# Kernel tuning notes

Measured on AMD Instinct MI355X. Metric: run time of the kernel, lower is better.

Reference implementation:

```python
import jax, jax.numpy as jnp
import numpy as np

B, T, S = 4, 128, 8192
HID, NH, NKV, HD = 2560, 8, 4, 256
INTER = 10240
WINDOW = 1024
SOFTCAP = 50.0
SCALING = 256 ** -0.5  # query_pre_attn_scalar ** -0.5
EPS = 1e-6
NEG = -2.3819763e38  # large negative for masking (matches Gemma mask value)
ROPE_THETA = 10000.0


def _rmsnorm(x, w):
    xf = x.astype(jnp.float32)
    o = xf * jax.lax.rsqrt(jnp.mean(xf * xf, axis=-1, keepdims=True) + EPS)
    return (o * (1.0 + w.astype(jnp.float32))).astype(x.dtype)


def _rope(x, cos, sin):
    # split-half rotation, matching torch apply_rotary_emb (chunk->complex->mul)
    d2 = x.shape[-1] // 2
    x1, x2 = x[..., :d2], x[..., d2:]
    c = cos[None, :, None, :]  # [1,T,1,D/2]
    s = sin[None, :, None, :]
    return jnp.concatenate([x1 * c - x2 * s, x1 * s + x2 * c], axis=-1)


def setup_inputs() -> dict:
    key = jax.random.key(0)
    ks = jax.random.split(key, 14)
    hidden_states = jax.random.normal(ks[0], (B, T, HID), jnp.float32)
    kv_write_indices = jnp.arange(T, dtype=jnp.int32)
    k_cache = jnp.zeros((B, S, NKV, HD), jnp.float32)
    v_cache = jnp.zeros((B, S, NKV, HD), jnp.float32)
    # rotary tables for positions 0..T-1
    inv = 1.0 / (ROPE_THETA ** (np.arange(0, HD, 2)[: HD // 2].astype(np.float32) / HD))
    fr = np.outer(np.arange(T, dtype=np.float32), inv).astype(np.float32)
    freqs_cos = jnp.asarray(np.cos(fr))
    freqs_sin = jnp.asarray(np.sin(fr))
    # masks: query i sits at absolute position i; cache slots >= T are unwritten
    qpos = jnp.arange(T)[:, None]
    kpos = jnp.arange(S)[None, :]
    causal = kpos <= qpos
    local = causal & ((qpos - kpos) < WINDOW)
    mask = jnp.broadcast_to(jnp.where(causal, 0.0, NEG)[None, None], (B, 1, T, S)).astype(jnp.float32)
    local_mask = jnp.broadcast_to(jnp.where(local, 0.0, NEG)[None, None], (B, 1, T, S)).astype(jnp.float32)
    sc = 0.02
    w_qkv = sc * jax.random.normal(ks[1], ((NH + 2 * NKV) * HD, HID), jnp.float32)
    w_o = sc * jax.random.normal(ks[2], (HID, NH * HD), jnp.float32)
    q_norm_w = 0.1 * jax.random.normal(ks[3], (HD,), jnp.float32)
    k_norm_w = 0.1 * jax.random.normal(ks[4], (HD,), jnp.float32)
    in_ln_w = 0.1 * jax.random.normal(ks[5], (HID,), jnp.float32)
    post_attn_ln_w = 0.1 * jax.random.normal(ks[6], (HID,), jnp.float32)
    pre_ffw_ln_w = 0.1 * jax.random.normal(ks[7], (HID,), jnp.float32)
    post_ffw_ln_w = 0.1 * jax.random.normal(ks[8], (HID,), jnp.float32)
    w_gate = sc * jax.random.normal(ks[9], (INTER, HID), jnp.float32)
    w_up = sc * jax.random.normal(ks[10], (INTER, HID), jnp.float32)
    w_down = sc * jax.random.normal(ks[11], (HID, INTER), jnp.float32)
    return {
        "hidden_states": hidden_states, "freqs_cos": freqs_cos, "freqs_sin": freqs_sin,
        "kv_write_indices": kv_write_indices, "k_cache": k_cache, "v_cache": v_cache,
        "mask": mask, "local_mask": local_mask,
        "w_qkv": w_qkv, "w_o": w_o, "q_norm_w": q_norm_w, "k_norm_w": k_norm_w,
        "in_ln_w": in_ln_w, "post_attn_ln_w": post_attn_ln_w,
        "pre_ffw_ln_w": pre_ffw_ln_w, "post_ffw_ln_w": post_ffw_ln_w,
        "w_gate": w_gate, "w_up": w_up, "w_down": w_down,
    }


def reference(hidden_states, freqs_cos, freqs_sin, kv_write_indices, k_cache, v_cache,
              mask, local_mask, w_qkv, w_o, q_norm_w, k_norm_w, in_ln_w,
              post_attn_ln_w, pre_ffw_ln_w, post_ffw_ln_w, w_gate, w_up, w_down):
    b, t, _ = hidden_states.shape
    residual = hidden_states
    h = _rmsnorm(hidden_states, in_ln_w)
    qkv = h @ w_qkv.T
    q_sz, kv_sz = NH * HD, NKV * HD
    xq = qkv[..., :q_sz].reshape(b, t, NH, HD)
    xk = qkv[..., q_sz:q_sz + kv_sz].reshape(b, t, NKV, HD)
    xv = qkv[..., q_sz + kv_sz:].reshape(b, t, NKV, HD)
    xq = _rmsnorm(xq, q_norm_w)  # QK-norm
    xk = _rmsnorm(xk, k_norm_w)
    xq = _rope(xq, freqs_cos, freqs_sin)
    xk = _rope(xk, freqs_cos, freqs_sin)
    kc = k_cache.at[:, kv_write_indices].set(xk)  # index_copy_ on dim 1
    vc = v_cache.at[:, kv_write_indices].set(xv)
    g = NH // NKV
    q = (xq * SCALING).reshape(b, t, NKV, g, HD)
    # GQA without repeat_interleave: group dim g shares each kv head
    scores = jnp.einsum('btkgd,bskd->bkgts', q, kc)
    scores = SOFTCAP * jnp.tanh(scores / SOFTCAP)  # logit softcapping
    scores = scores + local_mask[:, :, None]  # LOCAL_SLIDING -> use local mask
    probs = jax.nn.softmax(scores.astype(jnp.float32), axis=-1).astype(q.dtype)
    attn = jnp.einsum('bkgts,bskd->btkgd', probs, vc).reshape(b, t, NH * HD)
    attn = attn @ w_o.T
    h = residual + _rmsnorm(attn, post_attn_ln_w)
    residual = h
    x = _rmsnorm(h, pre_ffw_ln_w)
    gate = jax.nn.gelu(x @ w_gate.T, approximate=True)
    mlp = (gate * (x @ w_up.T)) @ w_down.T
    return residual + _rmsnorm(mlp, post_ffw_ln_w)
```

## Files before the change

kernel.cpp:

```cpp
#include <hip/hip_runtime.h>
#include <hip/hip_bf16.h>

#define B_ 4
#define T_ 128
#define HID 2560
#define NH 8
#define NKV 4
#define HD 256
#define INTER 10240
#define MROWS 512
#define EPS 1e-6f

typedef float f32x4 __attribute__((ext_vector_type(4)));
typedef __bf16 bf16x8 __attribute__((ext_vector_type(8)));

__device__ __forceinline__ unsigned short f2bf(float f){
  unsigned int u = __builtin_bit_cast(unsigned int, f);
  u += 0x7fffu + ((u >> 16) & 1u);
  return (unsigned short)(u >> 16);
}
__device__ __forceinline__ float bf2f(unsigned short u){
  unsigned int x = ((unsigned int)u) << 16;
  return __builtin_bit_cast(float, x);
}
__device__ __forceinline__ unsigned int cvtpk(float lo, float hi){
  unsigned int r;
  asm("v_cvt_pk_bf16_f32 %0, %1, %2" : "=v"(r) : "v"(lo), "v"(hi));
  return r;
}

__device__ __forceinline__ float bsum256(float v, float* buf){
  #pragma unroll
  for (int o = 32; o; o >>= 1) v += __shfl_xor(v, o);
  __syncthreads();
  if ((threadIdx.x & 63) == 0) buf[threadIdx.x >> 6] = v;
  __syncthreads();
  return buf[0] + buf[1] + buf[2] + buf[3];
}

__global__ __launch_bounds__(256) void rms_in(
    const float* __restrict__ x, const float* __restrict__ w,
    unsigned short* __restrict__ out)
{
  __shared__ float buf[4];
  const int r = blockIdx.x, tid = threadIdx.x;
  const float* xp = x + (size_t)r * HID;
  float v[10]; float ss = 0.f;
  #pragma unroll
  for (int j = 0; j < 10; j++){ v[j] = xp[tid + j*256]; ss += v[j]*v[j]; }
  ss = bsum256(ss, buf);
  float s = rsqrtf(ss * (1.f/HID) + EPS);
  #pragma unroll
  for (int j = 0; j < 10; j++){
    int i = tid + j*256;
    out[(size_t)r*HID + i] = f2bf(v[j] * s * (1.f + w[i]));
  }
}

template<bool BF16OUT>
__global__ __launch_bounds__(256, 2) void gemm_big(
    const unsigned short* __restrict__ A,
    const float* __restrict__ B0,
    const float* __restrict__ B1,
    int n_hi,
    void* __restrict__ Cv,
    int N, int K, int klen)
{
  __shared__ unsigned short As[2][256][40];
  __shared__ unsigned short Bs[2][128][40];
  const int tid = threadIdx.x;
  const int bid = (blockIdx.x & 7) * ((int)gridDim.x >> 3) + (blockIdx.x >> 3);
  const int bm = (bid & 1) << 8;
  const int bn = (bid >> 1) << 7;
  const int k0 = blockIdx.y * klen;
  const int nt = klen >> 5;

  const int srow = tid >> 1, shalf = tid & 1;
  const size_t A128 = (size_t)128 * K;
  const unsigned short* ApG = A + (size_t)(bm + srow) * K + k0 + (shalf << 4);
  const float* Bb = (bn < n_hi) ? B0 : B1;
  const int bnr = (bn < n_hi) ? bn : (bn - n_hi);
  const float* BpG = Bb + (size_t)(bnr + srow) * K + k0 + (shalf << 4);

  const int wave = tid >> 6, lane = tid & 63;
  const int wm = (wave & 1) << 7;
  const int wn = (wave >> 1) << 6;
  const int fr = lane & 15, kq = lane >> 4;

  f32x4 acc[8][4];
  #pragma unroll
  for (int i = 0; i < 8; i++)
    #pragma unroll
    for (int j = 0; j < 4; j++)
      #pragma unroll
      for (int e = 0; e < 4; e++) acc[i][j][e] = 0.f;

  uint4  ra0 = *(const uint4*)(ApG);
  uint4  ra1 = *(const uint4*)(ApG + 8);
  uint4  ra2 = *(const uint4*)(ApG + A128);
  uint4  ra3 = *(const uint4*)(ApG + A128 + 8);
  float4 rb0 = *(const float4*)(BpG);
  float4 rb1 = *(const float4*)(BpG + 4);
  float4 rb2 = *(const float4*)(BpG + 8);
  float4 rb3 = *(const float4*)(BpG + 12);

  int cur = 0;
  for (int t = 0; t < nt; t++) {
    uint4 w0, w1;
    w0.x = cvtpk(rb0.x, rb0.y); w0.y = cvtpk(rb0.z, rb0.w);
    w0.z = cvtpk(rb1.x, rb1.y); w0.w = cvtpk(rb1.z, rb1.w);
    w1.x = cvtpk(rb2.x, rb2.y); w1.y = cvtpk(rb2.z, rb2.w);
    w1.z = cvtpk(rb3.x, rb3.y); w1.w = cvtpk(rb3.z, rb3.w);
    *(uint4*)&As[cur][srow      ][(shalf<<4)]     = ra0;
    *(uint4*)&As[cur][srow      ][(shalf<<4) + 8] = ra1;
    *(uint4*)&As[cur][srow + 128][(shalf<<4)]     = ra2;
    *(uint4*)&As[cur][srow + 128][(shalf<<4) + 8] = ra3;
    *(uint4*)&Bs[cur][srow][(shalf<<4)]     = w0;
    *(uint4*)&Bs[cur][srow][(shalf<<4) + 8] = w1;
    __syncthreads();
    if (t + 1 < nt) {
      const unsigned short* a2 = ApG + ((t + 1) << 5);
      const float*          b2 = BpG + ((t + 1) << 5);
      ra0 = *(const uint4*)(a2);
      ra1 = *(const uint4*)(a2 + 8);
      ra2 = *(const uint4*)(a2 + A128);
      ra3 = *(const uint4*)(a2 + A128 + 8);
      rb0 = *(const float4*)(b2);
      rb1 = *(const float4*)(b2 + 4);
      rb2 = *(const float4*)(b2 + 8);
      rb3 = *(const float4*)(b2 + 12);
    }
    bf16x8 af[8], bfv[4];
    #pragma unroll
    for (int mi = 0; mi < 8; mi++) af[mi]  = *(const bf16x8*)&As[cur][wm + mi*16 + fr][kq*8];
    #pragma unroll
    for (int ni = 0; ni < 4; ni++) bfv[ni] = *(const bf16x8*)&Bs[cur][wn + ni*16 + fr][kq*8];
    #pragma unroll
    for (int mi = 0; mi < 8; mi++)
      #pragma unroll
      for (int ni = 0; ni < 4; ni++)
        acc[mi][ni] = __builtin_amdgcn_mfma_f32_16x16x32_bf16(af[mi], bfv[ni], acc[mi][ni], 0, 0, 0);
    cur ^= 1;
  }

  #pragma unroll
  for (int mi = 0; mi < 8; mi++) {
    #pragma unroll
    for (int ni = 0; ni < 4; ni++) {
      int m = bm + wm + mi*16 + kq*4;
      int n = bn + wn + ni*16 + fr;
      if (BF16OUT) {
        unsigned short* Cp = (unsigned short*)Cv + (size_t)blockIdx.y * MROWS * N;
        #pragma unroll
        for (int i = 0; i < 4; i++)
          Cp[(size_t)(m + i) * N + n] = f2bf(acc[mi][ni][i]);
      } else {
        float* Cp = (float*)Cv + (size_t)blockIdx.y * MROWS * N;
        #pragma unroll
        for (int i = 0; i < 4; i++)
          Cp[(size_t)(m + i) * N + n] = acc[mi][ni][i];
      }
    }
  }
}

__global__ __launch_bounds__(64) void qkv_post(
    const float* __restrict__ qkvp,
    const float* __restrict__ fcos, const float* __restrict__ fsin,
    const float* __restrict__ qnw, const float* __restrict__ knw,
    float* __restrict__ qout, float* __restrict__ kT, float* __restrict__ vout)
{
  const int row = blockIdx.x;
  const int hh  = blockIdx.y;
  const int b = row >> 7, t = row & 127;
  const int l = threadIdx.x;
  const size_t MS = (size_t)MROWS * 4096;
  const float* src = qkvp + (size_t)row * 4096 + hh * 256;
  float x[4];
  #pragma unroll
  for (int j = 0; j < 4; j++){
    int d = l + j*64;
    x[j] = src[d] + src[d + MS] + src[d + 2*MS] + src[d + 3*MS];
  }
  if (hh >= 12) {
    float* vp = vout + ((size_t)(b*NKV + (hh-12)) * T_ + t) * HD;
    #pragma unroll
    for (int j = 0; j < 4; j++) vp[l + j*64] = x[j];
    return;
  }
  float ss = x[0]*x[0] + x[1]*x[1] + x[2]*x[2] + x[3]*x[3];
  #pragma unroll
  for (int o = 32; o; o >>= 1) ss += __shfl_xor(ss, o);
  float r = rsqrtf(ss * (1.f/HD) + EPS);
  const float* nw = (hh < 8) ? qnw : knw;
  #pragma unroll
  for (int j = 0; j < 4; j++){ int d = l + j*64; x[j] = x[j] * r * (1.f + nw[d]); }
  float c0 = fcos[t*128 + l],      s0 = fsin[t*128 + l];
  float c1 = fcos[t*128 + l + 64], s1 = fsin[t*128 + l + 64];
  float y0 = x[0]*c0 - x[2]*s0;
  float y2 = x[0]*s0 + x[2]*c0;
  float y1 = x[1]*c1 - x[3]*s1;
  float y3 = x[1]*s1 + x[3]*c1;
  if (hh < 8) {
    float* qp = qout + ((size_t)(b*NH + hh) * T_ + t) * HD;
    const float sc = 0.0625f;
    qp[l] = y0*sc; qp[l+64] = y1*sc; qp[l+128] = y2*sc; qp[l+192] = y3*sc;
  } else {
    float* kp = kT + (size_t)(b*NKV + (hh-8)) * HD * T_;
    kp[(size_t)(l)*T_ + t] = y0;  kp[(size_t)(l+64)*T_ + t] = y1;
    kp[(size_t)(l+128)*T_ + t] = y2; kp[(size_t)(l+192)*T_ + t] = y3;
  }
}

__global__ __launch_bounds__(128) void attn_fwd(
    const float* __restrict__ q, const float* __restrict__ kT,
    const float* __restrict__ V, unsigned short* __restrict__ attn_out)
{
  const int id = blockIdx.x;
  const int t = id & 127;
  const int h = (id >> 7) & 7;
  const int b = id >> 10;
  const int kvh = h >> 1;
  const int tid = threadIdx.x;
  __shared__ float qs[256];
  __shared__ float sc[128];
  __shared__ float red[128];
  const float* qp = q + (size_t)id * HD;
  qs[tid] = qp[tid]; qs[tid + 128] = qp[tid + 128];
  __syncthreads();
  const float* kp = kT + (size_t)(b*NKV + kvh) * HD * T_;
  float dot = 0.f;
  const bool valid = (tid <= t);
  if (valid) {
    #pragma unroll 8
    for (int d = 0; d < 256; d++) dot += qs[d] * kp[(size_t)d*T_ + tid];
  }
  float score = valid ? 50.f * tanhf(dot * 0.02f) : -3.0e38f;
  sc[tid] = score; red[tid] = score;
  __syncthreads();
  for (int o = 64; o; o >>= 1){ if (tid < o) red[tid] = fmaxf(red[tid], red[tid+o]); __syncthreads(); }
  float m = red[0];
  __syncthreads();
  float p = valid ? __expf(score - m) : 0.f;
  sc[tid] = p; red[tid] = p;
  __syncthreads();
  for (int o = 64; o; o >>= 1){ if (tid < o) red[tid] += red[tid+o]; __syncthreads(); }
  float inv = 1.f / red[0];
  const float* vp = V + (size_t)(b*NKV + kvh) * T_ * HD;
  float a0 = 0.f, a1 = 0.f;
  for (int s = 0; s <= t; s++){
    float ps = sc[s];
    a0 += ps * vp[(size_t)s*HD + tid];
    a1 += ps * vp[(size_t)s*HD + tid + 128];
  }
  size_t orow = ((size_t)(b*T_ + t)) * 2048 + h * 256;
  attn_out[orow + tid]       = f2bf(a0 * inv);
  attn_out[orow + tid + 128] = f2bf(a1 * inv);
}

__global__ __launch_bounds__(256) void post_attn_k(
    const float* __restrict__ op, const float* __restrict__ hs,
    const float* __restrict__ wpost, const float* __restrict__ wpre,
    float* __restrict__ h2, unsigned short* __restrict__ xout)
{
  __shared__ float buf[4];
  const int r = blockIdx.x, tid = threadIdx.x;
  const size_t MS = (size_t)MROWS * HID;
  float o[10]; float ss = 0.f;
  #pragma unroll
  for (int j = 0; j < 10; j++){
    size_t i = (size_t)r*HID + tid + j*256;
    float v = 0.f;
    #pragma unroll
    for (int s = 0; s < 8; s++) v += op[i + s*MS];
    o[j] = v; ss += v*v;
  }
  ss = bsum256(ss, buf);
  float s = rsqrtf(ss*(1.f/HID) + EPS);
  float h[10]; float s2 = 0.f;
  #pragma unroll
  for (int j = 0; j < 10; j++){
    int i = tid + j*256;
    float hv = hs[(size_t)r*HID + i] + o[j]*s*(1.f + wpost[i]);
    h[j] = hv; h2[(size_t)r*HID + i] = hv; s2 += hv*hv;
  }
  s2 = bsum256(s2, buf);
  float sc2 = rsqrtf(s2*(1.f/HID) + EPS);
  #pragma unroll
  for (int j = 0; j < 10; j++){
    int i = tid + j*256;
    xout[(size_t)r*HID + i] = f2bf(h[j]*sc2*(1.f + wpre[i]));
  }
}

__global__ __launch_bounds__(256) void act_fuse(
    const unsigned short* __restrict__ gu,
    unsigned short* __restrict__ act)
{
  const int r = blockIdx.x;
  const size_t MS = (size_t)MROWS * 20480;
  const unsigned short* rowp = gu + (size_t)r * 20480;
  for (int c = threadIdx.x; c < INTER; c += 256){
    float g = 0.f, u = 0.f;
    #pragma unroll
    for (int s = 0; s < 4; s++){
      g += bf2f(rowp[s*MS + c]);
      u += bf2f(rowp[s*MS + c + INTER]);
    }
    float tt = tanhf(0.7978845608f * (g + 0.044715f * g*g*g));
    float ge = 0.5f * g * (1.f + tt);
    act[(size_t)r*INTER + c] = f2bf(ge * u);
  }
}

__global__ __launch_bounds__(256) void final_k(
    const float* __restrict__ dp, const float* __restrict__ h2,
    const float* __restrict__ w, float* __restrict__ out)
{
  __shared__ float buf[4];
  const int r = blockIdx.x, tid = threadIdx.x;
  const size_t MS = (size_t)MROWS * HID;
  float m[10]; float ss = 0.f;
  #pragma unroll
  for (int j = 0; j < 10; j++){
    size_t i = (size_t)r*HID + tid + j*256;
    float v = 0.f;
    #pragma unroll
    for (int s = 0; s < 8; s++) v += dp[i + s*MS];
    m[j] = v; ss += v*v;
  }
  ss = bsum256(ss, buf);
  float s = rsqrtf(ss*(1.f/HID) + EPS);
  #pragma unroll
  for (int j = 0; j < 10; j++){
    int i = tid + j*256;
    out[(size_t)r*HID + i] = h2[(size_t)r*HID + i] + m[j]*s*(1.f + w[i]);
  }
}

extern "C" void kernel_launch(void* const* d_in, const int* in_sizes, int n_in,
                              void* d_out, int out_size, void* d_ws, size_t ws_size,
                              hipStream_t stream)
{
  const float* hs     = (const float*)d_in[0];
  const float* fcos   = (const float*)d_in[1];
  const float* fsin   = (const float*)d_in[2];
  const float* w_qkv  = (const float*)d_in[8];
  const float* w_o    = (const float*)d_in[9];
  const float* qnw    = (const float*)d_in[10];
  const float* knw    = (const float*)d_in[11];
  const float* in_ln  = (const float*)d_in[12];
  const float* w_post = (const float*)d_in[13];
  const float* w_pre  = (const float*)d_in[14];
  const float* w_pffw = (const float*)d_in[15];
  const float* w_gate = (const float*)d_in[16];
  const float* w_up   = (const float*)d_in[17];
  const float* w_down = (const float*)d_in[18];
  float* out = (float*)d_out;

  char* p = (char*)d_ws;
  auto alloc = [&](size_t bytes)->void*{ void* r = p; p += (bytes + 255) & ~(size_t)255; return r; };
  void* P0 = alloc((size_t)4*MROWS*20480*2);
  void* P1 = alloc((size_t)8*MROWS*HID*4);
  unsigned short* h_b   = (unsigned short*)alloc((size_t)MROWS*HID*2);
  float* qbuf           = (float*)alloc((size_t)B_*NH*T_*HD*4);
  float* kT             = (float*)alloc((size_t)B_*NKV*HD*T_*4);
  float* vbuf           = (float*)alloc((size_t)B_*NKV*T_*HD*4);
  unsigned short* att_b = (unsigned short*)alloc((size_t)MROWS*2048*2);
  float* h2             = (float*)alloc((size_t)MROWS*HID*4);
  unsigned short* x_b   = (unsigned short*)alloc((size_t)MROWS*HID*2);
  unsigned short* act_b = (unsigned short*)alloc((size_t)MROWS*INTER*2);

  float* qkv_p          = (float*)P0;
  unsigned short* gu_p  = (unsigned short*)P0;
  float* o_p            = (float*)P1;
  float* down_p         = (float*)P1;

  rms_in<<<MROWS, 256, 0, stream>>>(hs, in_ln, h_b);
  gemm_big<false><<<dim3(64, 4), 256, 0, stream>>>(h_b, w_qkv, w_qkv, 1<<30, qkv_p, 4096, 2560, 640);
  qkv_post<<<dim3(MROWS, 16), 64, 0, stream>>>(qkv_p, fcos, fsin, qnw, knw, qbuf, kT, vbuf);
  attn_fwd<<<B_*NH*T_, 128, 0, stream>>>(qbuf, kT, vbuf, att_b);
  gemm_big<false><<<dim3(40, 8), 256, 0, stream>>>(att_b, w_o, w_o, 1<<30, o_p, 2560, 2048, 256);
  post_attn_k<<<MROWS, 256, 0, stream>>>(o_p, hs, w_post, w_pre, h2, x_b);
  gemm_big<true><<<dim3(320, 4), 256, 0, stream>>>(x_b, w_gate, w_up, 10240, gu_p, 20480, 2560, 640);
  act_fuse<<<MROWS, 256, 0, stream>>>(gu_p, act_b);
  gemm_big<false><<<dim3(40, 8), 256, 0, stream>>>(act_b, w_down, w_down, 1<<30, down_p, 2560, 10240, 1280);
  final_k<<<MROWS, 256, 0, stream>>>(down_p, h2, w_pffw, out);
}
```

Before: 399.5 us.

## Stage GEMM A tiles via direct global-to-LDS loads with triple buffering

The big GEMM's A-operand tiles are now copied straight from global memory into LDS with global_load_lds, into a three-deep buffer ring with an XOR swizzle on the rows. This replaces the old path that went through registers and then an LDS store. The fp32 B weights still go through registers for bf16 conversion, but are now prefetched two tiles ahead and double-buffered in LDS. MFMA issue is wrapped in s_setprio, and the minimum-occupancy hint is dropped from launch bounds. The goal is to cut register pressure and VALU/LDS-store work, and to hide more load latency. The risks are LDS capacity pressure and reliance on implicit vmcnt ordering to make the direct-to-LDS copies visible before use.

```diff
diff --git a/kernel.cpp b/kernel.cpp
--- a/kernel.cpp
+++ b/kernel.cpp
@@ -28,6 +28,11 @@
   asm("v_cvt_pk_bf16_f32 %0, %1, %2" : "=v"(r) : "v"(lo), "v"(hi));
   return r;
 }
+__device__ __forceinline__ void glds16(const void* g, void* l){
+  __builtin_amdgcn_global_load_lds(
+      (const __attribute__((address_space(1))) void*)g,
+      (__attribute__((address_space(3))) void*)l, 16, 0, 0);
+}
 
 __device__ __forceinline__ float bsum256(float v, float* buf){
   #pragma unroll
@@ -58,7 +63,7 @@
 }
 
 template<bool BF16OUT>
-__global__ __launch_bounds__(256, 2) void gemm_big(
+__global__ __launch_bounds__(256) void gemm_big(
     const unsigned short* __restrict__ A,
     const float* __restrict__ B0,
     const float* __restrict__ B1,
@@ -66,8 +71,8 @@
     void* __restrict__ Cv,
     int N, int K, int klen)
 {
-  __shared__ unsigned short As[2][256][40];
-  __shared__ unsigned short Bs[2][128][40];
+  __shared__ char AsRaw[3 * 16384];
+  __shared__ unsigned short Bs[2][128 * 40];
   const int tid = threadIdx.x;
   const int bid = (blockIdx.x & 7) * ((int)gridDim.x >> 3) + (blockIdx.x >> 3);
   const int bm = (bid & 1) << 8;
@@ -75,17 +80,17 @@
   const int k0 = blockIdx.y * klen;
   const int nt = klen >> 5;
 
+  const int w = tid >> 6, l = tid & 63;
   const int srow = tid >> 1, shalf = tid & 1;
-  const size_t A128 = (size_t)128 * K;
-  const unsigned short* ApG = A + (size_t)(bm + srow) * K + k0 + (shalf << 4);
+
   const float* Bb = (bn < n_hi) ? B0 : B1;
   const int bnr = (bn < n_hi) ? bn : (bn - n_hi);
   const float* BpG = Bb + (size_t)(bnr + srow) * K + k0 + (shalf << 4);
 
-  const int wave = tid >> 6, lane = tid & 63;
-  const int wm = (wave & 1) << 7;
-  const int wn = (wave >> 1) << 6;
-  const int fr = lane & 15, kq = lane >> 4;
+  const int wm = (w & 1) << 7;
+  const int wn = (w >> 1) << 6;
+  const int fr = l & 15, kq = l >> 4;
+  const int aslot = ((kq ^ ((fr >> 1) & 3)) << 4);
 
   f32x4 acc[8][4];
   #pragma unroll
@@ -95,52 +100,67 @@
       #pragma unroll
       for (int e = 0; e < 4; e++) acc[i][j][e] = 0.f;
 
-  uint4  ra0 = *(const uint4*)(ApG);
-  uint4  ra1 = *(const uint4*)(ApG + 8);
-  uint4  ra2 = *(const uint4*)(ApG + A128);
-  uint4  ra3 = *(const uint4*)(ApG + A128 + 8);
-  float4 rb0 = *(const float4*)(BpG);
-  float4 rb1 = *(const float4*)(BpG + 4);
-  float4 rb2 = *(const float4*)(BpG + 8);
-  float4 rb3 = *(const float4*)(BpG + 12);
-
-  int cur = 0;
-  for (int t = 0; t < nt; t++) {
+  auto STAGE_A = [&](int tt, int buf){
+    char* base = AsRaw + buf * 16384 + (w << 12);
+    const int koff = k0 + (tt << 5);
+    #pragma unroll
+    for (int c = 0; c < 4; c++){
+      int r = (w << 6) + (c << 4) + (l >> 2);
+      int j = (l & 3) ^ ((r >> 1) & 3);
+      const unsigned short* src = A + (size_t)(bm + r) * K + koff + (j << 3);
+      glds16(src, base + (c << 10));
+    }
+  };
+
+  float4 rb0, rb1, rb2, rb3;
+  auto LOAD_B = [&](int tt){
+    const float* b2 = BpG + (tt << 5);
+    rb0 = *(const float4*)(b2);
+    rb1 = *(const float4*)(b2 + 4);
+    rb2 = *(const float4*)(b2 + 8);
+    rb3 = *(const float4*)(b2 + 12);
+  };
+  auto CVT_WRITE_B = [&](int buf){
     uint4 w0, w1;
     w0.x = cvtpk(rb0.x, rb0.y); w0.y = cvtpk(rb0.z, rb0.w);
     w0.z = cvtpk(rb1.x, rb1.y); w0.w = cvtpk(rb1.z, rb1.w);
     w1.x = cvtpk(rb2.x, rb2.y); w1.y = cvtpk(rb2.z, rb2.w);
     w1.z = cvtpk(rb3.x, rb3.y); w1.w = cvtpk(rb3.z, rb3.w);
-    *(uint4*)&As[cur][srow      ][(shalf<<4)]     = ra0;
-    *(uint4*)&As[cur][srow      ][(shalf<<4) + 8] = ra1;
-    *(uint4*)&As[cur][srow + 128][(shalf<<4)]     = ra2;
-    *(uint4*)&As[cur][srow + 128][(shalf<<4) + 8] = ra3;
-    *(uint4*)&Bs[cur][srow][(shalf<<4)]     = w0;
-    *(uint4*)&Bs[cur][srow][(shalf<<4) + 8] = w1;
-    __syncthreads();
-    if (t + 1 < nt) {
-      const unsigned short* a2 = ApG + ((t + 1) << 5);
-      const float*          b2 = BpG + ((t + 1) << 5);
-      ra0 = *(const uint4*)(a2);
-      ra1 = *(const uint4*)(a2 + 8);
-      ra2 = *(const uint4*)(a2 + A128);
-      ra3 = *(const uint4*)(a2 + A128 + 8);
-      rb0 = *(const float4*)(b2);
-      rb1 = *(const float4*)(b2 + 4);
-      rb2 = *(const float4*)(b2 + 8);
-      rb3 = *(const float4*)(b2 + 12);
-    }
+    *(uint4*)&Bs[buf][srow * 40 + (shalf << 4)]     = w0;
+    *(uint4*)&Bs[buf][srow * 40 + (shalf << 4) + 8] = w1;
+  };
+
+  STAGE_A(0, 0);
+  STAGE_A(1, 1);
+  LOAD_B(0);
+  CVT_WRITE_B(0);
+  LOAD_B(1);
+  asm volatile("s_waitcnt lgkmcnt(0)" ::: "memory");
+  __builtin_amdgcn_s_barrier();
+
+  int ab = 0;
+  for (int t = 0; t < nt; t++) {
+    if (t + 2 < nt) STAGE_A(t + 2, (ab + 2 >= 3) ? ab - 1 : ab + 2);
+    const char* abp = AsRaw + ab * 16384;
     bf16x8 af[8], bfv[4];
     #pragma unroll
-    for (int mi = 0; mi < 8; mi++) af[mi]  = *(const bf16x8*)&As[cur][wm + mi*16 + fr][kq*8];
-    #pragma unroll
-    for (int ni = 0; ni < 4; ni++) bfv[ni] = *(const bf16x8*)&Bs[cur][wn + ni*16 + fr][kq*8];
+    for (int mi = 0; mi < 8; mi++)
+      af[mi] = *(const bf16x8*)(abp + ((wm + mi*16 + fr) << 6) + aslot);
+    #pragma unroll
+    for (int ni = 0; ni < 4; ni++)
+      bfv[ni] = *(const bf16x8*)&Bs[t & 1][(wn + ni*16 + fr) * 40 + kq * 8];
+    __builtin_amdgcn_s_setprio(1);
     #pragma unroll
     for (int mi = 0; mi < 8; mi++)
       #pragma unroll
       for (int ni = 0; ni < 4; ni++)
         acc[mi][ni] = __builtin_amdgcn_mfma_f32_16x16x32_bf16(af[mi], bfv[ni], acc[mi][ni], 0, 0, 0);
-    cur ^= 1;
+    __builtin_amdgcn_s_setprio(0);
+    if (t + 1 < nt) CVT_WRITE_B((t + 1) & 1);
+    if (t + 2 < nt) LOAD_B(t + 2);
+    asm volatile("s_waitcnt lgkmcnt(0)" ::: "memory");
+    __builtin_amdgcn_s_barrier();
+    ab = (ab + 1 >= 3) ? 0 : ab + 1;
   }
 
   #pragma unroll
```

Result: slower. 412.2 us (+3.2%).

## Replace LDS-tiled GEMM with register-streaming kernel covering all rows per block

Applied to the files above, without the earlier changes.

Rewrites the GEMM so each block covers all 512 rows and a 64-column slab. Each wave loads its A fragments and fp32 weights straight from global memory into registers, with no shared memory and no barriers. The fp32 weights are now read once instead of once per each of two M-tiles. The cost is that A is re-read by every block, so it depends on L2 to serve it. The QKV projection now uses 8-way split-K, and qkv_post sums eight partials to match.

```diff
diff --git a/kernel.cpp b/kernel.cpp
--- a/kernel.cpp
+++ b/kernel.cpp
@@ -58,7 +58,7 @@
 }
 
 template<bool BF16OUT>
-__global__ __launch_bounds__(256, 2) void gemm_big(
+__global__ __launch_bounds__(256, 2) void gemm_stream(
     const unsigned short* __restrict__ A,
     const float* __restrict__ B0,
     const float* __restrict__ B1,
@@ -66,26 +66,18 @@
     void* __restrict__ Cv,
     int N, int K, int klen)
 {
-  __shared__ unsigned short As[2][256][40];
-  __shared__ unsigned short Bs[2][128][40];
-  const int tid = threadIdx.x;
-  const int bid = (blockIdx.x & 7) * ((int)gridDim.x >> 3) + (blockIdx.x >> 3);
-  const int bm = (bid & 1) << 8;
-  const int bn = (bid >> 1) << 7;
+  const int bn = blockIdx.x << 6;
   const int k0 = blockIdx.y * klen;
   const int nt = klen >> 5;
 
-  const int srow = tid >> 1, shalf = tid & 1;
-  const size_t A128 = (size_t)128 * K;
-  const unsigned short* ApG = A + (size_t)(bm + srow) * K + k0 + (shalf << 4);
+  const int w = threadIdx.x >> 6, l = threadIdx.x & 63;
+  const int fr = l & 15, kq = l >> 4;
+
   const float* Bb = (bn < n_hi) ? B0 : B1;
-  const int bnr = (bn < n_hi) ? bn : (bn - n_hi);
-  const float* BpG = Bb + (size_t)(bnr + srow) * K + k0 + (shalf << 4);
-
-  const int wave = tid >> 6, lane = tid & 63;
-  const int wm = (wave & 1) << 7;
-  const int wn = (wave >> 1) << 6;
-  const int fr = lane & 15, kq = lane >> 4;
+  const int bnr = (bn < n_hi) ? bn : bn - n_hi;
+
+  const unsigned short* Ap = A + (size_t)(w*128 + fr) * K + k0 + kq*8;
+  const float*          Bp = Bb + (size_t)(bnr + fr) * K + k0 + kq*8;
 
   f32x4 acc[8][4];
   #pragma unroll
@@ -95,60 +87,52 @@
       #pragma unroll
       for (int e = 0; e < 4; e++) acc[i][j][e] = 0.f;
 
-  uint4  ra0 = *(const uint4*)(ApG);
-  uint4  ra1 = *(const uint4*)(ApG + 8);
-  uint4  ra2 = *(const uint4*)(ApG + A128);
-  uint4  ra3 = *(const uint4*)(ApG + A128 + 8);
-  float4 rb0 = *(const float4*)(BpG);
-  float4 rb1 = *(const float4*)(BpG + 4);
-  float4 rb2 = *(const float4*)(BpG + 8);
-  float4 rb3 = *(const float4*)(BpG + 12);
-
-  int cur = 0;
-  for (int t = 0; t < nt; t++) {
-    uint4 w0, w1;
-    w0.x = cvtpk(rb0.x, rb0.y); w0.y = cvtpk(rb0.z, rb0.w);
-    w0.z = cvtpk(rb1.x, rb1.y); w0.w = cvtpk(rb1.z, rb1.w);
-    w1.x = cvtpk(rb2.x, rb2.y); w1.y = cvtpk(rb2.z, rb2.w);
-    w1.z = cvtpk(rb3.x, rb3.y); w1.w = cvtpk(rb3.z, rb3.w);
-    *(uint4*)&As[cur][srow      ][(shalf<<4)]     = ra0;
-    *(uint4*)&As[cur][srow      ][(shalf<<4) + 8] = ra1;
-    *(uint4*)&As[cur][srow + 128][(shalf<<4)]     = ra2;
-    *(uint4*)&As[cur][srow + 128][(shalf<<4) + 8] = ra3;
-    *(uint4*)&Bs[cur][srow][(shalf<<4)]     = w0;
-    *(uint4*)&Bs[cur][srow][(shalf<<4) + 8] = w1;
-    __syncthreads();
-    if (t + 1 < nt) {
-      const unsigned short* a2 = ApG + ((t + 1) << 5);
-      const float*          b2 = BpG + ((t + 1) << 5);
-      ra0 = *(const uint4*)(a2);
-      ra1 = *(const uint4*)(a2 + 8);
-      ra2 = *(const uint4*)(a2 + A128);
-      ra3 = *(const uint4*)(a2 + A128 + 8);
-      rb0 = *(const float4*)(b2);
-      rb1 = *(const float4*)(b2 + 4);
-      rb2 = *(const float4*)(b2 + 8);
-      rb3 = *(const float4*)(b2 + 12);
-    }
-    bf16x8 af[8], bfv[4];
-    #pragma unroll
-    for (int mi = 0; mi < 8; mi++) af[mi]  = *(const bf16x8*)&As[cur][wm + mi*16 + fr][kq*8];
-    #pragma unroll
-    for (int ni = 0; ni < 4; ni++) bfv[ni] = *(const bf16x8*)&Bs[cur][wn + ni*16 + fr][kq*8];
+  float4 br[4][2];
+  #pragma unroll
+  for (int ni = 0; ni < 4; ni++){
+    const float* p = Bp + (size_t)(ni*16)*K;
+    br[ni][0] = *(const float4*)(p);
+    br[ni][1] = *(const float4*)(p + 4);
+  }
+
+  for (int t = 0; t < nt; t++){
+    uint4 ar[8];
     #pragma unroll
     for (int mi = 0; mi < 8; mi++)
+      ar[mi] = *(const uint4*)(Ap + (size_t)(mi*16)*K + t*32);
+    bf16x8 bfv[4];
+    #pragma unroll
+    for (int ni = 0; ni < 4; ni++){
+      union { unsigned int u[4]; bf16x8 v; } pk;
+      pk.u[0] = cvtpk(br[ni][0].x, br[ni][0].y);
+      pk.u[1] = cvtpk(br[ni][0].z, br[ni][0].w);
+      pk.u[2] = cvtpk(br[ni][1].x, br[ni][1].y);
+      pk.u[3] = cvtpk(br[ni][1].z, br[ni][1].w);
+      bfv[ni] = pk.v;
+    }
+    if (t + 1 < nt){
+      #pragma unroll
+      for (int ni = 0; ni < 4; ni++){
+        const float* p = Bp + (size_t)(ni*16)*K + (t+1)*32;
+        br[ni][0] = *(const float4*)(p);
+        br[ni][1] = *(const float4*)(p + 4);
+      }
+    }
+    #pragma unroll
+    for (int mi = 0; mi < 8; mi++){
+      bf16x8 af = __builtin_bit_cast(bf16x8, ar[mi]);
       #pragma unroll
       for (int ni = 0; ni < 4; ni++)
-        acc[mi][ni] = __builtin_amdgcn_mfma_f32_16x16x32_bf16(af[mi], bfv[ni], acc[mi][ni], 0, 0, 0);
-    cur ^= 1;
+        acc[mi][ni] = __builtin_amdgcn_mfma_f32_16x16x32_bf16(af, bfv[ni], acc[mi][ni], 0, 0, 0);
+    }
   }
 
   #pragma unroll
   for (int mi = 0; mi < 8; mi++) {
     #pragma unroll
     for (int ni = 0; ni < 4; ni++) {
-      int m = bm + wm + mi*16 + kq*4;
-      int n = bn + wn + ni*16 + fr;
+      int m = w*128 + mi*16 + kq*4;
+      int n = bn + ni*16 + fr;
       if (BF16OUT) {
         unsigned short* Cp = (unsigned short*)Cv + (size_t)blockIdx.y * MROWS * N;
         #pragma unroll
@@ -180,7 +164,10 @@
   #pragma unroll
   for (int j = 0; j < 4; j++){
     int d = l + j*64;
-    x[j] = src[d] + src[d + MS] + src[d + 2*MS] + src[d + 3*MS];
+    float v = 0.f;
+    #pragma unroll
+    for (int s = 0; s < 8; s++) v += src[d + s*MS];
+    x[j] = v;
   }
   if (hh >= 12) {
     float* vp = vout + ((size_t)(b*NKV + (hh-12)) * T_ + t) * HD;
@@ -377,13 +364,13 @@
   float* down_p         = (float*)P1;
 
   rms_in<<<MROWS, 256, 0, stream>>>(hs, in_ln, h_b);
-  gemm_big<false><<<dim3(64, 4), 256, 0, stream>>>(h_b, w_qkv, w_qkv, 1<<30, qkv_p, 4096, 2560, 640);
+  gemm_stream<false><<<dim3(64, 8), 256, 0, stream>>>(h_b, w_qkv, w_qkv, 1<<30, qkv_p, 4096, 2560, 320);
   qkv_post<<<dim3(MROWS, 16), 64, 0, stream>>>(qkv_p, fcos, fsin, qnw, knw, qbuf, kT, vbuf);
   attn_fwd<<<B_*NH*T_, 128, 0, stream>>>(qbuf, kT, vbuf, att_b);
-  gemm_big<false><<<dim3(40, 8), 256, 0, stream>>>(att_b, w_o, w_o, 1<<30, o_p, 2560, 2048, 256);
+  gemm_stream<false><<<dim3(40, 8), 256, 0, stream>>>(att_b, w_o, w_o, 1<<30, o_p, 2560, 2048, 256);
   post_attn_k<<<MROWS, 256, 0, stream>>>(o_p, hs, w_post, w_pre, h2, x_b);
-  gemm_big<true><<<dim3(320, 4), 256, 0, stream>>>(x_b, w_gate, w_up, 10240, gu_p, 20480, 2560, 640);
+  gemm_stream<true><<<dim3(320, 4), 256, 0, stream>>>(x_b, w_gate, w_up, 10240, gu_p, 20480, 2560, 640);
   act_fuse<<<MROWS, 256, 0, stream>>>(gu_p, act_b);
-  gemm_big<false><<<dim3(40, 8), 256, 0, stream>>>(act_b, w_down, w_down, 1<<30, down_p, 2560, 10240, 1280);
+  gemm_stream<false><<<dim3(40, 8), 256, 0, stream>>>(act_b, w_down, w_down, 1<<30, down_p, 2560, 10240, 1280);
   final_k<<<MROWS, 256, 0, stream>>>(down_p, h2, w_pffw, out);
 }
```

Result: slower. 596.8 us (+49.4%).

## Swizzle GEMM LDS tiles and deepen register prefetch to two stages

Applied to the files above, without the earlier changes.

Replaces the padded LDS tiles with unpadded 64-byte rows and an XOR swizzle on the 16-byte chunk index, to avoid bank conflicts without wasting shared memory. The main loop is unrolled by two with two register sets, so global loads run two tiles ahead of compute. MFMA sections are also raised in wave priority with s_setprio. This costs extra registers under launch_bounds(256,2) and assumes an even tile count per K split.

```diff
diff --git a/kernel.cpp b/kernel.cpp
--- a/kernel.cpp
+++ b/kernel.cpp
@@ -66,8 +66,8 @@
     void* __restrict__ Cv,
     int N, int K, int klen)
 {
-  __shared__ unsigned short As[2][256][40];
-  __shared__ unsigned short Bs[2][128][40];
+  __shared__ char As[2][256*64];
+  __shared__ char Bs[2][128*64];
   const int tid = threadIdx.x;
   const int bid = (blockIdx.x & 7) * ((int)gridDim.x >> 3) + (blockIdx.x >> 3);
   const int bm = (bid & 1) << 8;
@@ -86,6 +86,10 @@
   const int wm = (wave & 1) << 7;
   const int wn = (wave >> 1) << 6;
   const int fr = lane & 15, kq = lane >> 4;
+  const int aslot = ((kq ^ ((fr >> 1) & 3)) << 4);
+  const int arsw = (srow >> 1) & 3;
+  const int s0 = (((2*shalf)     ^ arsw) << 4);
+  const int s1 = (((2*shalf + 1) ^ arsw) << 4);
 
   f32x4 acc[8][4];
   #pragma unroll
@@ -95,53 +99,68 @@
       #pragma unroll
       for (int e = 0; e < 4; e++) acc[i][j][e] = 0.f;
 
-  uint4  ra0 = *(const uint4*)(ApG);
-  uint4  ra1 = *(const uint4*)(ApG + 8);
-  uint4  ra2 = *(const uint4*)(ApG + A128);
-  uint4  ra3 = *(const uint4*)(ApG + A128 + 8);
-  float4 rb0 = *(const float4*)(BpG);
-  float4 rb1 = *(const float4*)(BpG + 4);
-  float4 rb2 = *(const float4*)(BpG + 8);
-  float4 rb3 = *(const float4*)(BpG + 12);
-
-  int cur = 0;
-  for (int t = 0; t < nt; t++) {
-    uint4 w0, w1;
-    w0.x = cvtpk(rb0.x, rb0.y); w0.y = cvtpk(rb0.z, rb0.w);
-    w0.z = cvtpk(rb1.x, rb1.y); w0.w = cvtpk(rb1.z, rb1.w);
-    w1.x = cvtpk(rb2.x, rb2.y); w1.y = cvtpk(rb2.z, rb2.w);
-    w1.z = cvtpk(rb3.x, rb3.y); w1.w = cvtpk(rb3.z, rb3.w);
-    *(uint4*)&As[cur][srow      ][(shalf<<4)]     = ra0;
-    *(uint4*)&As[cur][srow      ][(shalf<<4) + 8] = ra1;
-    *(uint4*)&As[cur][srow + 128][(shalf<<4)]     = ra2;
-    *(uint4*)&As[cur][srow + 128][(shalf<<4) + 8] = ra3;
-    *(uint4*)&Bs[cur][srow][(shalf<<4)]     = w0;
-    *(uint4*)&Bs[cur][srow][(shalf<<4) + 8] = w1;
-    __syncthreads();
-    if (t + 1 < nt) {
-      const unsigned short* a2 = ApG + ((t + 1) << 5);
-      const float*          b2 = BpG + ((t + 1) << 5);
-      ra0 = *(const uint4*)(a2);
-      ra1 = *(const uint4*)(a2 + 8);
-      ra2 = *(const uint4*)(a2 + A128);
-      ra3 = *(const uint4*)(a2 + A128 + 8);
-      rb0 = *(const float4*)(b2);
-      rb1 = *(const float4*)(b2 + 4);
-      rb2 = *(const float4*)(b2 + 8);
-      rb3 = *(const float4*)(b2 + 12);
-    }
+  uint4 ra0, ra1, ra2, ra3; float4 rb0, rb1, rb2, rb3;
+  uint4 sa0, sa1, sa2, sa3; float4 sb0, sb1, sb2, sb3;
+
+#define LOAD_R(tt) { const unsigned short* ap = ApG + ((tt) << 5); const float* bp = BpG + ((tt) << 5); \
+  ra0 = *(const uint4*)(ap); ra1 = *(const uint4*)(ap + 8); \
+  ra2 = *(const uint4*)(ap + A128); ra3 = *(const uint4*)(ap + A128 + 8); \
+  rb0 = *(const float4*)(bp); rb1 = *(const float4*)(bp + 4); \
+  rb2 = *(const float4*)(bp + 8); rb3 = *(const float4*)(bp + 12); }
+#define LOAD_S(tt) { const unsigned short* ap = ApG + ((tt) << 5); const float* bp = BpG + ((tt) << 5); \
+  sa0 = *(const uint4*)(ap); sa1 = *(const uint4*)(ap + 8); \
+  sa2 = *(const uint4*)(ap + A128); sa3 = *(const uint4*)(ap + A128 + 8); \
+  sb0 = *(const float4*)(bp); sb1 = *(const float4*)(bp + 4); \
+  sb2 = *(const float4*)(bp + 8); sb3 = *(const float4*)(bp + 12); }
+#define WRITE_TILE(cur, a0,a1,a2,a3, b0,b1,b2,b3) { \
+  char* abase = &As[cur][srow*64]; \
+  *(uint4*)(abase + s0) = a0; \
+  *(uint4*)(abase + s1) = a1; \
+  *(uint4*)(abase + 128*64 + s0) = a2; \
+  *(uint4*)(abase + 128*64 + s1) = a3; \
+  uint4 w0, w1; \
+  w0.x = cvtpk(b0.x,b0.y); w0.y = cvtpk(b0.z,b0.w); \
+  w0.z = cvtpk(b1.x,b1.y); w0.w = cvtpk(b1.z,b1.w); \
+  w1.x = cvtpk(b2.x,b2.y); w1.y = cvtpk(b2.z,b2.w); \
+  w1.z = cvtpk(b3.x,b3.y); w1.w = cvtpk(b3.z,b3.w); \
+  char* bbase = &Bs[cur][srow*64]; \
+  *(uint4*)(bbase + s0) = w0; \
+  *(uint4*)(bbase + s1) = w1; }
+
+  auto COMPUTE = [&](int cur){
+    const char* ab = As[cur];
+    const char* bb = Bs[cur];
     bf16x8 af[8], bfv[4];
     #pragma unroll
-    for (int mi = 0; mi < 8; mi++) af[mi]  = *(const bf16x8*)&As[cur][wm + mi*16 + fr][kq*8];
-    #pragma unroll
-    for (int ni = 0; ni < 4; ni++) bfv[ni] = *(const bf16x8*)&Bs[cur][wn + ni*16 + fr][kq*8];
+    for (int mi = 0; mi < 8; mi++)
+      af[mi] = *(const bf16x8*)(ab + ((wm + mi*16 + fr) << 6) + aslot);
+    #pragma unroll
+    for (int ni = 0; ni < 4; ni++)
+      bfv[ni] = *(const bf16x8*)(bb + ((wn + ni*16 + fr) << 6) + aslot);
+    __builtin_amdgcn_s_setprio(1);
     #pragma unroll
     for (int mi = 0; mi < 8; mi++)
       #pragma unroll
       for (int ni = 0; ni < 4; ni++)
         acc[mi][ni] = __builtin_amdgcn_mfma_f32_16x16x32_bf16(af[mi], bfv[ni], acc[mi][ni], 0, 0, 0);
-    cur ^= 1;
-  }
+    __builtin_amdgcn_s_setprio(0);
+  };
+
+  LOAD_R(0);
+  LOAD_S(1);
+  for (int t = 0; t < nt; t += 2) {
+    WRITE_TILE(0, ra0,ra1,ra2,ra3, rb0,rb1,rb2,rb3);
+    __syncthreads();
+    if (t + 2 < nt) LOAD_R(t + 2);
+    COMPUTE(0);
+    WRITE_TILE(1, sa0,sa1,sa2,sa3, sb0,sb1,sb2,sb3);
+    __syncthreads();
+    if (t + 3 < nt) LOAD_S(t + 3);
+    COMPUTE(1);
+  }
+#undef LOAD_R
+#undef LOAD_S
+#undef WRITE_TILE
 
   #pragma unroll
   for (int mi = 0; mi < 8; mi++) {
```

Result: faster. 369.7 us (-7.5%).
